# Performance work log

Measured on AMD Instinct MI355X. Metric: run time of the kernel, lower is better.

Reference implementation:

```python
import jax, jax.numpy as jnp
import numpy as np

N_WORDS = 8192   # total words across all concepts
L = 24           # chars per word (padded)
D = 256          # word_vec_d
H = 8            # attention heads
DFF = 1024
VOCAB = 128
N_CONCEPTS = 1024
MAXW = 16        # max_words
GROUPS = 4       # n_names: 4 equal groups of concepts


def setup_inputs() -> dict:
    key = jax.random.key(0)
    ks = jax.random.split(key, 9)
    rng = np.random.default_rng(0)
    # char tokens in [1, VOCAB), ragged word lengths in [4, L], tail = 0 (pad)
    vals = rng.integers(1, VOCAB, size=(N_WORDS, L))
    lens = rng.integers(4, L + 1, size=(N_WORDS,))
    inputs = np.where(np.arange(L)[None, :] < lens[:, None], vals, 0)
    # ragged words-per-concept: alternate 4 / 12 -> sums to N_WORDS, <= MAXW
    counts = np.where(np.arange(N_CONCEPTS) % 2 == 0, 4, 12)
    concept_id = np.repeat(np.arange(N_CONCEPTS), counts)
    word_pos = np.concatenate([np.arange(c) for c in counts])

    def w(k, shape):
        return 0.02 * jax.random.normal(k, shape, jnp.float32)

    return {
        "inputs": jnp.asarray(inputs, jnp.int32),
        "concept_id": jnp.asarray(concept_id, jnp.int32),
        "word_pos": jnp.asarray(word_pos, jnp.int32),
        "n_concepts": N_CONCEPTS,
        "n_names": GROUPS,
        "we_emb": w(ks[0], (VOCAB, D)),
        "we_qkv": w(ks[1], (D, 3 * D)),
        "we_o": w(ks[2], (D, D)),
        "we_ff1": w(ks[3], (D, DFF)),
        "we_ff2": w(ks[4], (DFF, D)),
        "ne_qkv": w(ks[5], (D, 3 * D)),
        "ne_o": w(ks[6], (D, D)),
        "ne_ff1": w(ks[7], (D, DFF)),
        "ne_ff2": w(ks[8], (DFF, D)),
    }


def _ln(x):
    m = x.mean(-1, keepdims=True)
    v = ((x - m) ** 2).mean(-1, keepdims=True)
    return (x - m) * jax.lax.rsqrt(v + 1e-5)


def _mha(x, wqkv, wo, key_pad=None):
    n, l, d = x.shape
    hd = d // H
    q, k, v = jnp.split(x @ wqkv, 3, axis=-1)
    q = q.reshape(n, l, H, hd)
    k = k.reshape(n, l, H, hd)
    v = v.reshape(n, l, H, hd)
    s = jnp.einsum('nqhd,nkhd->nhqk', q, k) / jnp.sqrt(jnp.asarray(hd, x.dtype))
    if key_pad is not None:
        s = jnp.where(key_pad[:, None, None, :], -1e9, s)
    a = jax.nn.softmax(s, axis=-1)
    o = jnp.einsum('nhqk,nkhd->nqhd', a, v).reshape(n, l, d)
    return o @ wo


def _block(x, wqkv, wo, w1, w2, key_pad=None):
    h = _ln(x + _mha(x, wqkv, wo, key_pad))
    return _ln(h + jax.nn.relu(h @ w1) @ w2)


def reference(inputs, concept_id, word_pos, n_concepts, n_names,
              we_emb, we_qkv, we_o, we_ff1, we_ff2,
              ne_qkv, ne_o, ne_ff1, ne_ff2):
    pad_mask = inputs == 0  # [N_WORDS, L]
    x = we_emb[inputs]      # [N_WORDS, L, D]
    word_ft = _block(x, we_qkv, we_o, we_ff1, we_ff2, pad_mask)
    # masked mean over chars -> one vector per word
    np_mask = (~pad_mask)[..., None].astype(word_ft.dtype)  # [N_WORDS, L, 1]
    name_vec = (word_ft * np_mask).sum(1) / np_mask.sum(1)   # [N_WORDS, D]
    # ragged -> padded: one scatter instead of per-sample torch.cat
    padded = jnp.zeros((n_concepts, MAXW, name_vec.shape[-1]), name_vec.dtype)
    padded = padded.at[concept_id, word_pos].set(name_vec)   # [n_concepts, MAXW, D]
    name_ft = _block(padded, ne_qkv, ne_o, ne_ff1, ne_ff2)
    row_pad = (padded == 0).all(-1, keepdims=True)           # all-zero rows = pad words
    name_ft = jnp.where(row_pad, jnp.zeros((), name_ft.dtype), name_ft)
    counts = (name_ft != 0).sum(1).astype(name_ft.dtype)     # [n_concepts, D]
    pooled = name_ft.sum(1) / counts                         # [n_concepts, D]
    return tuple(jnp.split(pooled, n_names, axis=0))
```

## Files before the change

kernel.cpp:

```cpp
#include <hip/hip_runtime.h>
#include <hip/hip_bf16.h>

#define NWORDS 8192
#define LW 24
#define DIM 256
#define NHEAD 8
#define DFF 1024
#define NCONC 1024
#define MAXW 16
#define TN (NCONC * MAXW)

typedef float floatx4 __attribute__((ext_vector_type(4)));
typedef short shortx8 __attribute__((ext_vector_type(8)));

__device__ __forceinline__ float bf2f(ushort u) {
  union { uint u; float f; } v; v.u = ((uint)u) << 16; return v.f;
}
__device__ __forceinline__ ushort f2bf(float f) {
  union { float f; uint u; } v; v.f = f;
  return (ushort)((v.u + 0x7FFFu + ((v.u >> 16) & 1u)) >> 16);
}

__device__ __forceinline__ void load_lds16(const ushort* gsrc, ushort* lds) {
  __builtin_amdgcn_global_load_lds((const __attribute__((address_space(1))) void*)gsrc,
                                   (__attribute__((address_space(3))) void*)lds, 16, 0, 0);
}

#define WAIT_VM0() __builtin_amdgcn_s_waitcnt(0x0F70)
#define WAIT_LGKM0() __builtin_amdgcn_s_waitcnt(0xC07F)

#define STAGE_COL(lane) ((((lane) & 3) ^ (((lane) >> 3) & 3)) * 8)
#define FRAG_OFF(row, quad) (((row) * 32) + ((((quad) ^ (((row) >> 1) & 3))) * 8))

__global__ __launch_bounds__(256) void wprep(const float* __restrict__ W,
                                             ushort* __restrict__ WT, int K, int N) {
  int idx = blockIdx.x * 256 + threadIdx.x;
  if (idx < K * N) {
    int k = idx / N, n = idx % N;
    WT[n * K + k] = f2bf(W[idx]);
  }
}

__global__ __launch_bounds__(256) void embed4(const int* __restrict__ inputs,
                                              const float* __restrict__ we_emb,
                                              ushort* __restrict__ x, int ntok) {
  int idx = blockIdx.x * 256 + threadIdx.x;
  int t = idx >> 6, d = (idx & 63) * 4;
  if (t < ntok) {
    const float4 f = *(const float4*)&we_emb[inputs[t] * DIM + d];
    uint2 o;
    o.x = (uint)f2bf(f.x) | ((uint)f2bf(f.y) << 16);
    o.y = (uint)f2bf(f.z) | ((uint)f2bf(f.w) << 16);
    *(uint2*)&x[(size_t)t * DIM + d] = o;
  }
}

template <bool LN>
__global__ __launch_bounds__(256, 2) void gemm_tok64(const ushort* __restrict__ A, int lda,
                                                     const ushort* __restrict__ BT,
                                                     const ushort* __restrict__ RES,
                                                     ushort* __restrict__ C, int ldc) {
  __shared__ __align__(16) ushort As[8 * 64 * 32];
  __shared__ __align__(16) ushort Wb[256 * 32];
  __shared__ float red1[64 * 4];
  __shared__ float red2[64 * 4];
  const int tid = threadIdx.x;
  const int w = tid >> 6, lane = tid & 63;
  const int quad = lane >> 4, l16 = lane & 15;
  const long m0 = (long)blockIdx.y * 64;
  const long nb = (long)blockIdx.x * 256;
  const int srow = lane >> 2;
  const int scol = STAGE_COL(lane);
  const int wc = w * 64;

#pragma unroll
  for (int t = 0; t < 8; t++) {
    int p = 2 * w + t / 4, ii = t % 4;
    load_lds16(&A[(m0 + ii * 16 + srow) * lda + p * 32 + scol], &As[p * 2048 + (ii * 16) * 32]);
  }
#pragma unroll
  for (int ii = 0; ii < 4; ii++)
    load_lds16(&BT[(nb + wc + ii * 16 + srow) * 256 + scol], &Wb[(wc + ii * 16) * 32]);
  __syncthreads();

  floatx4 acc[4][4] = {};
#pragma unroll 1
  for (int p = 0; p < 8; p++) {
    WAIT_VM0();
    shortx8 a[4], b[4];
#pragma unroll
    for (int j = 0; j < 4; j++)
      b[j] = *(const shortx8*)&Wb[FRAG_OFF(wc + j * 16 + l16, quad)];
    WAIT_LGKM0();
    if (p < 7) {
#pragma unroll
      for (int ii = 0; ii < 4; ii++)
        load_lds16(&BT[(nb + wc + ii * 16 + srow) * 256 + (p + 1) * 32 + scol],
                   &Wb[(wc + ii * 16) * 32]);
    }
#pragma unroll
    for (int i = 0; i < 4; i++)
      a[i] = *(const shortx8*)&As[p * 2048 + FRAG_OFF(i * 16 + l16, quad)];
#pragma unroll
    for (int i = 0; i < 4; i++)
#pragma unroll
      for (int j = 0; j < 4; j++)
        acc[i][j] = __builtin_amdgcn_mfma_f32_16x16x32_bf16(a[i], b[j], acc[i][j], 0, 0, 0);
  }

  if (!LN) {
#pragma unroll
    for (int i = 0; i < 4; i++)
#pragma unroll
      for (int j = 0; j < 4; j++)
#pragma unroll
        for (int r = 0; r < 4; r++) {
          long m = m0 + i * 16 + quad * 4 + r;
          C[m * ldc + nb + wc + j * 16 + l16] = f2bf(acc[i][j][r]);
        }
    return;
  }

#pragma unroll
  for (int i = 0; i < 4; i++)
#pragma unroll
    for (int r = 0; r < 4; r++) {
      int row = i * 16 + quad * 4 + r;
      float s1 = 0.f, s2 = 0.f;
#pragma unroll
      for (int j = 0; j < 4; j++) {
        float v = acc[i][j][r] + bf2f(RES[(m0 + row) * 256 + wc + j * 16 + l16]);
        acc[i][j][r] = v;
        s1 += v;
        s2 += v * v;
      }
#pragma unroll
      for (int off = 1; off < 16; off <<= 1) {
        s1 += __shfl_xor(s1, off);
        s2 += __shfl_xor(s2, off);
      }
      if (l16 == 0) { red1[row * 4 + w] = s1; red2[row * 4 + w] = s2; }
    }
  __syncthreads();
#pragma unroll
  for (int i = 0; i < 4; i++)
#pragma unroll
    for (int r = 0; r < 4; r++) {
      int row = i * 16 + quad * 4 + r;
      float s1 = red1[row * 4] + red1[row * 4 + 1] + red1[row * 4 + 2] + red1[row * 4 + 3];
      float s2 = red2[row * 4] + red2[row * 4 + 1] + red2[row * 4 + 2] + red2[row * 4 + 3];
      float mean = s1 * (1.f / 256.f);
      float rstd = rsqrtf(s2 * (1.f / 256.f) - mean * mean + 1e-5f);
#pragma unroll
      for (int j = 0; j < 4; j++)
        C[(m0 + row) * 256 + wc + j * 16 + l16] = f2bf((acc[i][j][r] - mean) * rstd);
    }
}

__global__ __launch_bounds__(256, 2) void ffn_fused(const ushort* __restrict__ H,
                                                    const ushort* __restrict__ W1T,
                                                    const ushort* __restrict__ W2T,
                                                    ushort* __restrict__ C,
                                                    int M) {
  __shared__ __align__(16) ushort As[8 * 64 * 32];
  __shared__ __align__(16) ushort Ss[8 * 64 * 32];
  __shared__ __align__(16) ushort Wb[256 * 32];
  const int tid = threadIdx.x;
  const int w = tid >> 6, lane = tid & 63;
  const int quad = lane >> 4, l16 = lane & 15;
  const long m0 = (long)blockIdx.x * 64;
  const int srow = lane >> 2;
  const int scol = STAGE_COL(lane);

#pragma unroll
  for (int t = 0; t < 8; t++) {
    int p = 2 * w + t / 4, ii = t % 4;
    load_lds16(&H[(m0 + ii * 16 + srow) * 256 + p * 32 + scol], &As[(p * 2048) + (ii * 16) * 32]);
  }
#pragma unroll
  for (int ii = 0; ii < 4; ii++)
    load_lds16(&W1T[(long)(w * 64 + ii * 16 + srow) * 256 + scol], &Wb[(w * 64 + ii * 16) * 32]);
  __syncthreads();

  floatx4 acc2[4][4] = {};
  for (int m = 0; m < 4; m++) {
    floatx4 acc1[4][4] = {};
    if (m > 0) {
#pragma unroll
      for (int ii = 0; ii < 4; ii++)
        load_lds16(&W1T[(long)(m * 256 + w * 64 + ii * 16 + srow) * 256 + scol],
                   &Wb[(w * 64 + ii * 16) * 32]);
    }
#pragma unroll 1
    for (int p = 0; p < 8; p++) {
      WAIT_VM0();
      shortx8 a[4], b[4];
#pragma unroll
      for (int i = 0; i < 4; i++)
        a[i] = *(const shortx8*)&Wb[FRAG_OFF(w * 64 + i * 16 + l16, quad)];
      WAIT_LGKM0();
      if (p < 7) {
#pragma unroll
        for (int ii = 0; ii < 4; ii++)
          load_lds16(&W1T[(long)(m * 256 + w * 64 + ii * 16 + srow) * 256 + (p + 1) * 32 + scol],
                     &Wb[(w * 64 + ii * 16) * 32]);
      }
#pragma unroll
      for (int j = 0; j < 4; j++)
        b[j] = *(const shortx8*)&As[p * 2048 + FRAG_OFF(j * 16 + l16, quad)];
#pragma unroll
      for (int i = 0; i < 4; i++)
#pragma unroll
        for (int j = 0; j < 4; j++)
          acc1[i][j] = __builtin_amdgcn_mfma_f32_16x16x32_bf16(a[i], b[j], acc1[i][j], 0, 0, 0);
    }
    __syncthreads();
#pragma unroll
    for (int i = 0; i < 4; i++) {
      int fb = w * 64 + i * 16 + quad * 4;
      int pf = fb >> 5, c = (fb >> 3) & 3, off = fb & 7;
#pragma unroll
      for (int j = 0; j < 4; j++) {
        int tok = j * 16 + l16;
        ushort4 pk;
        pk.x = f2bf(fmaxf(acc1[i][j][0], 0.f));
        pk.y = f2bf(fmaxf(acc1[i][j][1], 0.f));
        pk.z = f2bf(fmaxf(acc1[i][j][2], 0.f));
        pk.w = f2bf(fmaxf(acc1[i][j][3], 0.f));
        *(ushort4*)&Ss[(pf * 64 + tok) * 32 + ((c ^ ((tok >> 1) & 3)) << 3) + off] = pk;
      }
    }
    __syncthreads();
#pragma unroll
    for (int jj = 0; jj < 4; jj++)
      load_lds16(&W2T[(long)(w * 64 + jj * 16 + srow) * 1024 + m * 256 + scol],
                 &Wb[(w * 64 + jj * 16) * 32]);
#pragma unroll 1
    for (int p = 0; p < 8; p++) {
      WAIT_VM0();
      shortx8 a[4], b[4];
#pragma unroll
      for (int j = 0; j < 4; j++)
        b[j] = *(const shortx8*)&Wb[FRAG_OFF(w * 64 + j * 16 + l16, quad)];
      WAIT_LGKM0();
      if (p < 7) {
#pragma unroll
        for (int jj = 0; jj < 4; jj++)
          load_lds16(&W2T[(long)(w * 64 + jj * 16 + srow) * 1024 + m * 256 + (p + 1) * 32 + scol],
                     &Wb[(w * 64 + jj * 16) * 32]);
      }
#pragma unroll
      for (int i = 0; i < 4; i++)
        a[i] = *(const shortx8*)&Ss[p * 2048 + FRAG_OFF(i * 16 + l16, quad)];
#pragma unroll
      for (int i = 0; i < 4; i++)
#pragma unroll
        for (int j = 0; j < 4; j++)
          acc2[i][j] = __builtin_amdgcn_mfma_f32_16x16x32_bf16(a[i], b[j], acc2[i][j], 0, 0, 0);
    }
  }
  __syncthreads();

  float* red1 = (float*)Ss;
  float* red2 = red1 + 256;
  const int wc = w * 64;
#pragma unroll
  for (int i = 0; i < 4; i++)
#pragma unroll
    for (int r = 0; r < 4; r++) {
      int row = i * 16 + quad * 4 + r;
      float s1 = 0.f, s2 = 0.f;
#pragma unroll
      for (int j = 0; j < 4; j++) {
        float v = acc2[i][j][r] + bf2f(H[(m0 + row) * 256 + wc + j * 16 + l16]);
        acc2[i][j][r] = v;
        s1 += v;
        s2 += v * v;
      }
#pragma unroll
      for (int off = 1; off < 16; off <<= 1) {
        s1 += __shfl_xor(s1, off);
        s2 += __shfl_xor(s2, off);
      }
      if (l16 == 0) { red1[row * 4 + w] = s1; red2[row * 4 + w] = s2; }
    }
  __syncthreads();
#pragma unroll
  for (int i = 0; i < 4; i++)
#pragma unroll
    for (int r = 0; r < 4; r++) {
      int row = i * 16 + quad * 4 + r;
      float s1 = red1[row * 4] + red1[row * 4 + 1] + red1[row * 4 + 2] + red1[row * 4 + 3];
      float s2 = red2[row * 4] + red2[row * 4 + 1] + red2[row * 4 + 2] + red2[row * 4 + 3];
      float mean = s1 * (1.f / 256.f);
      float rstd = rsqrtf(s2 * (1.f / 256.f) - mean * mean + 1e-5f);
      if (m0 + row < M) {
#pragma unroll
        for (int j = 0; j < 4; j++)
          C[(m0 + row) * 256 + wc + j * 16 + l16] = f2bf((acc2[i][j][r] - mean) * rstd);
      }
    }
}

template <int LSEQ, bool MASKED>
__global__ __launch_bounds__(256) void attn(const int* __restrict__ inputs,
                                            ushort* __restrict__ qkv) {
  __shared__ ushort Qs[LSEQ * 256];
  __shared__ ushort Ks[LSEQ * 256];
  __shared__ ushort Vs[LSEQ * 256];
  __shared__ float pads[LSEQ];
  const int blk = blockIdx.x;
  const int tid = threadIdx.x;
  ushort* base = qkv + (size_t)blk * LSEQ * 768;
  const uint4* src = (const uint4*)base;
  for (int i = tid; i < LSEQ * 96; i += 256) {
    int c = i / 96, part = i % 96;
    uint4 val = src[c * 96 + part];
    int sect = part >> 5, off = part & 31;
    ushort* dst = (sect == 0) ? Qs : (sect == 1 ? Ks : Vs);
    *(uint4*)&dst[c * 256 + off * 8] = val;
  }
  if (MASKED) {
    if (tid < LSEQ) pads[tid] = (inputs[blk * LSEQ + tid] == 0) ? 1.f : 0.f;
  }
  __syncthreads();
  if (tid < LSEQ * NHEAD) {
    const int i = tid % LSEQ, hh = tid / LSEQ;
    const int hb = hh * 32;
    float q[32];
    {
      const uint4* qr = (const uint4*)&Qs[i * 256 + hb];
#pragma unroll
      for (int u = 0; u < 4; u++) {
        uint4 ch = qr[u];
        const ushort* us = (const ushort*)&ch;
#pragma unroll
        for (int d = 0; d < 8; d++) q[u * 8 + d] = bf2f(us[d]);
      }
    }
    float s[LSEQ];
    float mx = -3e38f;
#pragma unroll
    for (int j = 0; j < LSEQ; j++) {
      const uint4* kr = (const uint4*)&Ks[j * 256 + hb];
      float a = 0.f;
#pragma unroll
      for (int u = 0; u < 4; u++) {
        uint4 ch = kr[u];
        const ushort* us = (const ushort*)&ch;
#pragma unroll
        for (int d = 0; d < 8; d++) a += q[u * 8 + d] * bf2f(us[d]);
      }
      a *= 0.17677669529663687f;
      if (MASKED && pads[j] != 0.f) a = -1e9f;
      s[j] = a;
      mx = fmaxf(mx, a);
    }
    float den = 0.f;
#pragma unroll
    for (int j = 0; j < LSEQ; j++) { s[j] = __expf(s[j] - mx); den += s[j]; }
    float inv = 1.f / den;
    float o[32] = {};
#pragma unroll
    for (int j = 0; j < LSEQ; j++) {
      float a = s[j] * inv;
      const uint4* vr = (const uint4*)&Vs[j * 256 + hb];
#pragma unroll
      for (int u = 0; u < 4; u++) {
        uint4 ch = vr[u];
        const ushort* us = (const ushort*)&ch;
#pragma unroll
        for (int d = 0; d < 8; d++) o[u * 8 + d] += a * bf2f(us[d]);
      }
    }
    ushort* orow = base + (size_t)i * 768 + hb;
#pragma unroll
    for (int d = 0; d < 32; d++) orow[d] = f2bf(o[d]);
  }
}

__global__ __launch_bounds__(256) void pool_scatter(const ushort* __restrict__ ft,
                                                    const int* __restrict__ inputs,
                                                    const int* __restrict__ cid,
                                                    const int* __restrict__ wpos,
                                                    ushort* __restrict__ padded,
                                                    int* __restrict__ flags) {
  int w = blockIdx.x, d = threadIdx.x;
  float s = 0.f;
  int cnt = 0;
  for (int c = 0; c < LW; c++) {
    if (inputs[w * LW + c] != 0) {
      s += bf2f(ft[((size_t)w * LW + c) * DIM + d]);
      cnt++;
    }
  }
  int slot = cid[w] * MAXW + wpos[w];
  padded[(size_t)slot * DIM + d] = f2bf(s / (float)cnt);
  if (d == 0) flags[slot] = 1;
}

__global__ __launch_bounds__(256) void final_pool(const ushort* __restrict__ nft,
                                                  const int* __restrict__ flags,
                                                  float* __restrict__ out) {
  int n = blockIdx.x, d = threadIdx.x;
  float s = 0.f;
  int cnt = 0;
  for (int wd = 0; wd < MAXW; wd++) {
    if (flags[n * MAXW + wd]) {
      s += bf2f(nft[((size_t)n * MAXW + wd) * DIM + d]);
      cnt++;
    }
  }
  out[n * DIM + d] = s / (float)cnt;
}

extern "C" void kernel_launch(void* const* d_in, const int* in_sizes, int n_in,
                              void* d_out, int out_size, void* d_ws, size_t ws_size,
                              hipStream_t stream) {
  const int* inputs = (const int*)d_in[0];
  const int* cid = (const int*)d_in[1];
  const int* wpos = (const int*)d_in[2];
  const float* we_emb = (const float*)d_in[5];
  const float* we_qkv = (const float*)d_in[6];
  const float* we_o = (const float*)d_in[7];
  const float* we_ff1 = (const float*)d_in[8];
  const float* we_ff2 = (const float*)d_in[9];
  const float* ne_qkv = (const float*)d_in[10];
  const float* ne_o = (const float*)d_in[11];
  const float* ne_ff1 = (const float*)d_in[12];
  const float* ne_ff2 = (const float*)d_in[13];
  float* out = (float*)d_out;

  int chunks = 4;
  if (ws_size >= 515000000UL) chunks = 1;
  else if (ws_size >= 263258112UL) chunks = 2;
  const int wpc = NWORDS / chunks;
  const int tpc = wpc * LW;

  const size_t X = (size_t)tpc * DIM * 2;
  const size_t Q = (size_t)tpc * 768 * 2;

  char* base = (char*)d_ws;
  ushort* x = (ushort*)(base);
  ushort* qkv = (ushort*)(base + X);
  ushort* h = (ushort*)(base + X + Q);
  ushort* ft = qkv;
  size_t pend = X + Q + X;
  ushort* padded = (ushort*)(base + pend);
  int* flags = (int*)(base + pend + 8388608);
  ushort* wT = (ushort*)(base + pend + 8454144);
  ushort* nqkv = (ushort*)(base);
  ushort* nh = (ushort*)(base + 25165824);
  ushort* nft = (ushort*)(base + 33554432);

  ushort* wqkvT = wT;
  ushort* woT = wT + 196608;
  ushort* wff1T = wT + 262144;
  ushort* wff2T = wT + 524288;
  ushort* nqkvT = wT + 786432;
  ushort* neoT = wT + 983040;
  ushort* neff1T = wT + 1048576;
  ushort* neff2T = wT + 1310720;

  wprep<<<768, 256, 0, stream>>>(we_qkv, wqkvT, 256, 768);
  wprep<<<256, 256, 0, stream>>>(we_o, woT, 256, 256);
  wprep<<<1024, 256, 0, stream>>>(we_ff1, wff1T, 256, 1024);
  wprep<<<1024, 256, 0, stream>>>(we_ff2, wff2T, 1024, 256);
  wprep<<<768, 256, 0, stream>>>(ne_qkv, nqkvT, 256, 768);
  wprep<<<256, 256, 0, stream>>>(ne_o, neoT, 256, 256);
  wprep<<<1024, 256, 0, stream>>>(ne_ff1, neff1T, 256, 1024);
  wprep<<<1024, 256, 0, stream>>>(ne_ff2, neff2T, 1024, 256);

  (void)hipMemsetAsync(padded, 0, (size_t)TN * DIM * 2, stream);
  (void)hipMemsetAsync(flags, 0, TN * 4, stream);

  for (int c = 0; c < chunks; c++) {
    const int* in_c = inputs + (size_t)c * wpc * LW;
    const int* cid_c = cid + (size_t)c * wpc;
    const int* wpos_c = wpos + (size_t)c * wpc;

    embed4<<<tpc / 4, 256, 0, stream>>>(in_c, we_emb, x, tpc);
    {
      dim3 g(3, tpc / 64);
      gemm_tok64<false><<<g, 256, 0, stream>>>(x, 256, wqkvT, nullptr, qkv, 768);
    }
    attn<24, true><<<wpc, 256, 0, stream>>>(in_c, qkv);
    {
      dim3 g(1, tpc / 64);
      gemm_tok64<true><<<g, 256, 0, stream>>>(qkv, 768, woT, x, h, 256);
    }
    ffn_fused<<<tpc / 64, 256, 0, stream>>>(h, wff1T, wff2T, ft, tpc);
    pool_scatter<<<wpc, 256, 0, stream>>>(ft, in_c, cid_c, wpos_c, padded, flags);
  }

  {
    dim3 g(3, TN / 64);
    gemm_tok64<false><<<g, 256, 0, stream>>>(padded, 256, nqkvT, nullptr, nqkv, 768);
  }
  attn<16, false><<<NCONC, 256, 0, stream>>>(nullptr, nqkv);
  {
    dim3 g(1, TN / 64);
    gemm_tok64<true><<<g, 256, 0, stream>>>(nqkv, 768, neoT, padded, nh, 256);
  }
  ffn_fused<<<TN / 64, 256, 0, stream>>>(nh, neff1T, neff2T, nft, TN);
  final_pool<<<NCONC, 256, 0, stream>>>(nft, flags, out);
}
```

Baseline: 972.8 us.

## Rewrite per-sequence attention with MFMA bf16 tiles and swizzled LDS layouts

Replaces the scalar per-thread attention (one thread per query row and head, fp32 dot products over LDS) with wave-level MFMA 16x16x32 bf16 matmuls for QK^T and PV. Each wave handles two heads. Sequences are padded to 32 rows, and Q, K and transposed V are stored in LDS with XOR swizzles to avoid bank conflicts. Softmax runs on the MFMA accumulator layout using shuffle reductions, and probabilities are staged through LDS as bf16. This aims to cut ALU and LDS read cost in attention, at the price of padding waste for LSEQ=24/16, extra zero-fill, and bf16 rounding of the probabilities.

```diff
diff --git a/kernel.cpp b/kernel.cpp
--- a/kernel.cpp
+++ b/kernel.cpp
@@ -305,77 +305,142 @@
 template <int LSEQ, bool MASKED>
 __global__ __launch_bounds__(256) void attn(const int* __restrict__ inputs,
                                             ushort* __restrict__ qkv) {
-  __shared__ ushort Qs[LSEQ * 256];
-  __shared__ ushort Ks[LSEQ * 256];
-  __shared__ ushort Vs[LSEQ * 256];
-  __shared__ float pads[LSEQ];
+  __shared__ __align__(16) ushort Qs[32 * 256];
+  __shared__ __align__(16) ushort Ks[32 * 256];
+  __shared__ __align__(16) ushort Vt[256 * 32];
+  __shared__ __align__(16) ushort Ps[4 * 32 * 32];
+  __shared__ float pads[32];
+  constexpr int MT = (LSEQ + 15) / 16;
   const int blk = blockIdx.x;
   const int tid = threadIdx.x;
+  const int w = tid >> 6, lane = tid & 63;
+  const int quad = lane >> 4, l16 = lane & 15;
   ushort* base = qkv + (size_t)blk * LSEQ * 768;
   const uint4* src = (const uint4*)base;
+  const uint4 z4 = {0u, 0u, 0u, 0u};
+
+  for (int i = tid; i < (32 - LSEQ) * 32 * 2; i += 256) {
+    int arr = (i >= (32 - LSEQ) * 32);
+    int rem = arr ? i - (32 - LSEQ) * 32 : i;
+    int row = LSEQ + (rem >> 5), ch = rem & 31;
+    *(uint4*)&((arr ? Ks : Qs)[row * 256 + ch * 8]) = z4;
+  }
+  for (int i = tid; i < 256 * (4 - LSEQ / 8); i += 256) {
+    int row = i & 255, pc = LSEQ / 8 + (i >> 8);
+    *(uint4*)&Vt[row * 32 + ((pc ^ ((row >> 3) & 3)) * 8)] = z4;
+  }
+  {
+    ushort* pz = Ps + w * 1024;
+    *(uint4*)&pz[lane * 16] = z4;
+    *(uint4*)&pz[lane * 16 + 8] = z4;
+  }
+  if (tid < 32) {
+    float pv = 1.f;
+    if (tid < LSEQ) pv = MASKED ? ((inputs[blk * LSEQ + tid] == 0) ? 1.f : 0.f) : 0.f;
+    pads[tid] = pv;
+  }
   for (int i = tid; i < LSEQ * 96; i += 256) {
     int c = i / 96, part = i % 96;
     uint4 val = src[c * 96 + part];
     int sect = part >> 5, off = part & 31;
-    ushort* dst = (sect == 0) ? Qs : (sect == 1 ? Ks : Vs);
-    *(uint4*)&dst[c * 256 + off * 8] = val;
-  }
-  if (MASKED) {
-    if (tid < LSEQ) pads[tid] = (inputs[blk * LSEQ + tid] == 0) ? 1.f : 0.f;
+    if (sect == 0) {
+      *(uint4*)&Qs[c * 256 + ((off ^ (c & 7)) * 8)] = val;
+    } else if (sect == 1) {
+      *(uint4*)&Ks[c * 256 + ((off ^ (c & 7)) * 8)] = val;
+    } else {
+      int d0 = (off & 31) * 8;
+      const ushort* us = (const ushort*)&val;
+#pragma unroll
+      for (int j = 0; j < 8; j++) {
+        int dim = d0 + j;
+        Vt[dim * 32 + (((c >> 3) ^ ((dim >> 3) & 3)) * 8) + (c & 7)] = us[j];
+      }
+    }
   }
   __syncthreads();
-  if (tid < LSEQ * NHEAD) {
-    const int i = tid % LSEQ, hh = tid / LSEQ;
-    const int hb = hh * 32;
-    float q[32];
-    {
-      const uint4* qr = (const uint4*)&Qs[i * 256 + hb];
-#pragma unroll
-      for (int u = 0; u < 4; u++) {
-        uint4 ch = qr[u];
-        const ushort* us = (const ushort*)&ch;
-#pragma unroll
-        for (int d = 0; d < 8; d++) q[u * 8 + d] = bf2f(us[d]);
-      }
-    }
-    float s[LSEQ];
-    float mx = -3e38f;
-#pragma unroll
-    for (int j = 0; j < LSEQ; j++) {
-      const uint4* kr = (const uint4*)&Ks[j * 256 + hb];
-      float a = 0.f;
-#pragma unroll
-      for (int u = 0; u < 4; u++) {
-        uint4 ch = kr[u];
-        const ushort* us = (const ushort*)&ch;
-#pragma unroll
-        for (int d = 0; d < 8; d++) a += q[u * 8 + d] * bf2f(us[d]);
-      }
-      a *= 0.17677669529663687f;
-      if (MASKED && pads[j] != 0.f) a = -1e9f;
-      s[j] = a;
-      mx = fmaxf(mx, a);
-    }
-    float den = 0.f;
-#pragma unroll
-    for (int j = 0; j < LSEQ; j++) { s[j] = __expf(s[j] - mx); den += s[j]; }
-    float inv = 1.f / den;
-    float o[32] = {};
-#pragma unroll
-    for (int j = 0; j < LSEQ; j++) {
-      float a = s[j] * inv;
-      const uint4* vr = (const uint4*)&Vs[j * 256 + hb];
-#pragma unroll
-      for (int u = 0; u < 4; u++) {
-        uint4 ch = vr[u];
-        const ushort* us = (const ushort*)&ch;
-#pragma unroll
-        for (int d = 0; d < 8; d++) o[u * 8 + d] += a * bf2f(us[d]);
-      }
-    }
-    ushort* orow = base + (size_t)i * 768 + hb;
-#pragma unroll
-    for (int d = 0; d < 32; d++) orow[d] = f2bf(o[d]);
+
+  ushort* Psw = Ps + w * 1024;
+#pragma unroll
+  for (int t = 0; t < 2; t++) {
+    const int h = w * 2 + t, hb = h * 32;
+    shortx8 aq[MT], bk[MT];
+#pragma unroll
+    for (int i = 0; i < MT; i++)
+      aq[i] = *(const shortx8*)&Qs[(i * 16 + l16) * 256 + (((h * 4 + quad) ^ (l16 & 7)) * 8)];
+#pragma unroll
+    for (int j = 0; j < MT; j++)
+      bk[j] = *(const shortx8*)&Ks[(j * 16 + l16) * 256 + (((h * 4 + quad) ^ (l16 & 7)) * 8)];
+    floatx4 s[MT][MT];
+#pragma unroll
+    for (int i = 0; i < MT; i++)
+#pragma unroll
+      for (int j = 0; j < MT; j++) {
+        floatx4 zz = {0.f, 0.f, 0.f, 0.f};
+        s[i][j] = __builtin_amdgcn_mfma_f32_16x16x32_bf16(aq[i], bk[j], zz, 0, 0, 0);
+      }
+    float pv[MT];
+#pragma unroll
+    for (int j = 0; j < MT; j++) pv[j] = pads[j * 16 + l16];
+#pragma unroll
+    for (int i = 0; i < MT; i++) {
+#pragma unroll
+      for (int r = 0; r < 4; r++) {
+        float v[MT];
+        float mx = -3e38f;
+#pragma unroll
+        for (int j = 0; j < MT; j++) {
+          float x = s[i][j][r] * 0.17677669529663687f;
+          if (pv[j] != 0.f) x = -1e9f;
+          v[j] = x;
+          mx = fmaxf(mx, x);
+        }
+#pragma unroll
+        for (int off = 1; off < 16; off <<= 1) mx = fmaxf(mx, __shfl_xor(mx, off));
+        float den = 0.f;
+#pragma unroll
+        for (int j = 0; j < MT; j++) { v[j] = __expf(v[j] - mx); den += v[j]; }
+#pragma unroll
+        for (int off = 1; off < 16; off <<= 1) den += __shfl_xor(den, off);
+        float inv = 1.f / den;
+        int row = i * 16 + quad * 4 + r;
+#pragma unroll
+        for (int j = 0; j < MT; j++) {
+          int col = j * 16 + l16;
+          Psw[row * 32 + (((col >> 3) ^ ((row >> 1) & 3)) * 8) + (col & 7)] = f2bf(v[j] * inv);
+        }
+      }
+    }
+    WAIT_LGKM0();
+    shortx8 pa[MT], bv[2];
+#pragma unroll
+    for (int i = 0; i < MT; i++) {
+      int row = i * 16 + l16;
+      pa[i] = *(const shortx8*)&Psw[row * 32 + ((quad ^ ((row >> 1) & 3)) * 8)];
+    }
+#pragma unroll
+    for (int jj = 0; jj < 2; jj++) {
+      int row = hb + jj * 16 + l16;
+      bv[jj] = *(const shortx8*)&Vt[row * 32 + ((quad ^ ((row >> 3) & 3)) * 8)];
+    }
+    floatx4 o[MT][2];
+#pragma unroll
+    for (int i = 0; i < MT; i++)
+#pragma unroll
+      for (int jj = 0; jj < 2; jj++) {
+        floatx4 zz = {0.f, 0.f, 0.f, 0.f};
+        o[i][jj] = __builtin_amdgcn_mfma_f32_16x16x32_bf16(pa[i], bv[jj], zz, 0, 0, 0);
+      }
+#pragma unroll
+    for (int i = 0; i < MT; i++)
+#pragma unroll
+      for (int r = 0; r < 4; r++) {
+        int row = i * 16 + quad * 4 + r;
+        if (row < LSEQ) {
+#pragma unroll
+          for (int jj = 0; jj < 2; jj++)
+            base[(size_t)row * 768 + hb + jj * 16 + l16] = f2bf(o[i][jj][r]);
+        }
+      }
   }
 }
 
```

New measurement: 936.3 us. 3.7% less time.
